# Kernel tuning notes

Hardware: AMD Instinct MI355X
Metric: run time of the kernel (lower is better)

The kernel has to match this reference:

```python
import jax, jax.numpy as jnp
from jax import lax
import numpy as np

T, B = 64, 32            # rollout length, num envs
IMG = 84                 # NatureCNN input size
POS_N = 10               # grid size per position axis
N_ACT = 5                # discrete actions
HID = 128                # LSTM hidden size
CNN_OUT = 512
IN_DIM = CNN_OUT + 2 * POS_N  # 532


def setup_inputs() -> dict:
    key = jax.random.key(0)
    ks = jax.random.split(key, 16)
    N = T * B
    s = 0.05  # weight scale to keep activations in sane range
    rn = lambda k, shp: jax.random.normal(k, shp, jnp.float32) * s
    return {
        "image": jax.random.uniform(ks[0], (N, IMG, IMG, 3), jnp.float32),
        "position": jax.random.randint(ks[1], (N, 2), 0, POS_N, jnp.int32),
        "done": jax.random.randint(ks[2], (N,), 0, 2, jnp.int32),
        "h0": jnp.zeros((B, 1, HID), jnp.float32),
        "c0": jnp.zeros((B, 1, HID), jnp.float32),
        "W1": rn(ks[3], (8, 8, 3, 32)),   "b1": jnp.zeros((32,), jnp.float32),
        "W2": rn(ks[4], (4, 4, 32, 64)),  "b2": jnp.zeros((64,), jnp.float32),
        "W3": rn(ks[5], (3, 3, 64, 64)),  "b3": jnp.zeros((64,), jnp.float32),
        "Wfc": rn(ks[6], (3136, CNN_OUT)), "bfc": jnp.zeros((CNN_OUT,), jnp.float32),
        "Wih": rn(ks[7], (4 * HID, IN_DIM)), "Whh": rn(ks[8], (4 * HID, HID)),
        "bih": jnp.zeros((4 * HID,), jnp.float32), "bhh": jnp.zeros((4 * HID,), jnp.float32),
        "Wp": rn(ks[9], (HID, N_ACT)), "bp": jnp.zeros((N_ACT,), jnp.float32),
        "Wv": rn(ks[10], (HID, 1)),    "bv": jnp.zeros((1,), jnp.float32),
    }


def _conv(x, w, b, stride):
    y = lax.conv_general_dilated(x, w, (stride, stride), 'VALID',
                                 dimension_numbers=('NHWC', 'HWIO', 'NHWC'))
    return jax.nn.relu(y + b)


def reference(image, position, done, h0, c0,
              W1, b1, W2, b2, W3, b3, Wfc, bfc,
              Wih, Whh, bih, bhh, Wp, bp, Wv, bv):
    # --- NatureCNN feature extractor ---
    x = _conv(image, W1, b1, 4)          # (N,20,20,32)
    x = _conv(x, W2, b2, 2)              # (N,9,9,64)
    x = _conv(x, W3, b3, 1)              # (N,7,7,64)
    x = x.reshape(x.shape[0], -1)        # (N,3136)
    feat = jax.nn.relu(x @ Wfc + bfc)    # (N,512)
    # --- one-hot position encoding ---
    oh = jnp.concatenate([jax.nn.one_hot(position[:, 0], POS_N, dtype=feat.dtype),
                          jax.nn.one_hot(position[:, 1], POS_N, dtype=feat.dtype)], axis=1)
    z = jnp.concatenate([feat, oh], axis=1).reshape(T, B, IN_DIM)
    d = done.astype(feat.dtype).reshape(T, B)
    # --- per-timestep masked LSTM scan with episode resets ---
    h = h0[:, 0, :]  # (B,HID), num_layers=1
    c = c0[:, 0, :]

    def step(carry, inp):
        h, c = carry
        x_t, d_t = inp
        m = (1.0 - d_t)[:, None]
        h = h * m
        c = c * m
        g = x_t @ Wih.T + bih + h @ Whh.T + bhh          # (B,4*HID)
        i, f, gg, o = jnp.split(g, 4, axis=1)             # torch gate order i,f,g,o
        i = jax.nn.sigmoid(i)
        f = jax.nn.sigmoid(f)
        o = jax.nn.sigmoid(o)
        c = f * c + i * jnp.tanh(gg)
        h = o * jnp.tanh(c)
        return (h, c), h

    (h, c), hs = lax.scan(step, (h, c), (z, d))
    H = hs.reshape(T * B, HID)
    logits = H @ Wp + bp                 # (N, N_ACT) -> Categorical logits
    v = H @ Wv + bv                      # (N, 1)
    return logits, v, h[:, None, :], c[:, None, :]
```

## Files before the change

kernel.cpp:

```cpp
#include <hip/hip_runtime.h>

typedef unsigned short ushort_t;
typedef unsigned int uint_t;
typedef __attribute__((ext_vector_type(8))) short short8;
typedef __attribute__((ext_vector_type(4))) short short4v;
typedef __attribute__((ext_vector_type(4))) float floatx4;

__device__ __forceinline__ float bf2f(ushort_t u){
    union { uint_t i; float f; } c; c.i = ((uint_t)u) << 16; return c.f;
}
__device__ __forceinline__ ushort_t f2bf(float x){
    union { float f; uint_t i; } c; c.f = x;
    uint_t i = c.i;
    return (ushort_t)((i + 0x7fffu + ((i >> 16) & 1u)) >> 16);
}
__device__ __forceinline__ uint_t cvt2fast(float a, float b){
    union { float f; uint_t i; } ca, cb; ca.f = a; cb.f = b;
    uint_t ia = ca.i + 0x8000u, ib = cb.i + 0x8000u;
    return __builtin_amdgcn_perm(ib, ia, 0x07060302u);
}
__device__ __forceinline__ short8 lds_load8(const ushort_t* p){
    union { short4v h[2]; short8 s; } u;
    u.h[0] = *(const short4v*)p;
    u.h[1] = *(const short4v*)(p + 4);
    return u.s;
}
__device__ __forceinline__ float relu_f(float x){ return fmaxf(x, 0.0f); }
__device__ __forceinline__ float sigmoid_f(float x){ return 1.0f / (1.0f + __expf(-x)); }

#define NT 2048
#define TT 64

__global__ __launch_bounds__(256) void prep_kernel(
    const float* __restrict__ Wih, ushort_t* __restrict__ Wihb)
{
    int i = blockIdx.x * 256 + threadIdx.x;
    int j = i >> 9, k = i & 511;
    Wihb[i] = f2bf(Wih[j * 532 + k]);
}

__global__ __launch_bounds__(256) void prep_convw_kernel(
    const float* __restrict__ W1, const float* __restrict__ W2,
    const float* __restrict__ W3, ushort_t* __restrict__ W1b,
    ushort_t* __restrict__ W2b, ushort_t* __restrict__ W3b)
{
    int i = blockIdx.x * 256 + threadIdx.x;
    if (i < 8192) {
        int ky = i >> 10, oc = (i >> 5) & 31, k = i & 31;
        float v = 0.0f;
        if (k < 24) { int kx = k / 3, ic = k % 3; v = W1[((ky * 8 + kx) * 3 + ic) * 32 + oc]; }
        W1b[i] = f2bf(v);
        return;
    }
    i -= 8192;
    if (i < 32768) {
        int kk = i >> 11, oc = (i >> 5) & 63, ic = i & 31;
        W2b[i] = f2bf(W2[(kk * 32 + ic) * 64 + oc]);
        return;
    }
    i -= 32768;
    if (i < 36864) {
        int p = i >> 12, oc = (i >> 6) & 63, ic = i & 63;
        W3b[i] = f2bf(W3[(p * 64 + ic) * 64 + oc]);
    }
}

__global__ __launch_bounds__(256) void wfct_kernel(
    const float* __restrict__ Wfc, ushort_t* __restrict__ WfcT)
{
    __shared__ ushort_t t_s[64][65];
    int kb = blockIdx.x % 49, jb = blockIdx.x / 49;
    int k0 = kb * 64, j0 = jb * 64;
    int jj = threadIdx.x & 63, i4 = threadIdx.x >> 6;
    for (int rr = i4; rr < 64; rr += 4)
        t_s[rr][jj] = f2bf(Wfc[(size_t)(k0 + rr) * 512 + j0 + jj]);
    __syncthreads();
    for (int rr = i4; rr < 64; rr += 4)
        WfcT[(size_t)(j0 + rr) * 3136 + k0 + jj] = t_s[jj][rr];
}

__global__ __launch_bounds__(256) void convs_mfma(
    const float* __restrict__ img,
    const ushort_t* __restrict__ W1b, const float* __restrict__ b1,
    const ushort_t* __restrict__ W2b, const float* __restrict__ b2,
    const ushort_t* __restrict__ W3b, const float* __restrict__ b3,
    ushort_t* __restrict__ out3)
{
    __shared__ ushort_t smem[35576];
    ushort_t* c1_s  = smem;
    ushort_t* img_s = smem + 14400;
    ushort_t* c2_s  = smem + 14400;

    int n = blockIdx.x, tid = threadIdx.x;
    int w = tid >> 6, lane = tid & 63;
    int r = lane & 15, q = lane >> 4;

    const float4* ip = (const float4*)(img + (size_t)n * 21168);
    for (int i = tid; i < 5292; i += 256) {
        float4 v = ip[i];
        uint_t lo = cvt2fast(v.x, v.y);
        uint_t hi = cvt2fast(v.z, v.w);
        *(uint2*)(img_s + i * 4) = make_uint2(lo, hi);
    }
    if (tid < 8) img_s[21168 + tid] = 0;
    __syncthreads();

    {
        int oct = w & 1;
        short8 bf[8];
        #pragma unroll
        for (int ky = 0; ky < 8; ky++)
            bf[ky] = *(const short8*)(W1b + (ky * 32 + oct * 16 + r) * 32 + q * 8);
        float bb = b1[oct * 16 + r];
        for (int t = (w >> 1); t < 25; t += 2) {
            int pxa = t * 16 + r;
            int oy = pxa / 20, ox = pxa % 20;
            floatx4 acc = {0.f, 0.f, 0.f, 0.f};
            #pragma unroll
            for (int ky = 0; ky < 8; ky++) {
                short8 a = lds_load8(img_s + ((oy * 4 + ky) * 84 + ox * 4) * 3 + q * 8);
                acc = __builtin_amdgcn_mfma_f32_16x16x32_bf16(a, bf[ky], acc, 0, 0, 0);
            }
            int pxs = t * 16 + q * 4;
            #pragma unroll
            for (int i = 0; i < 4; i++)
                c1_s[(pxs + i) * 36 + oct * 16 + r] = f2bf(relu_f(acc[i] + bb));
        }
    }
    __syncthreads();

    {
        int oct = w;
        short8 bfr[16];
        #pragma unroll
        for (int kk = 0; kk < 16; kk++)
            bfr[kk] = *(const short8*)(W2b + (kk * 64 + oct * 16 + r) * 32 + q * 8);
        float bb = b2[oct * 16 + r];
        for (int t = 0; t < 6; t++) {
            int pxa = min(t * 16 + r, 80);
            int oy = pxa / 9, ox = pxa % 9;
            floatx4 acc = {0.f, 0.f, 0.f, 0.f};
            #pragma unroll
            for (int ky = 0; ky < 4; ky++) {
                #pragma unroll
                for (int kx = 0; kx < 4; kx++) {
                    int qin = (oy * 2 + ky) * 20 + ox * 2 + kx;
                    short8 a = lds_load8(c1_s + qin * 36 + q * 8);
                    acc = __builtin_amdgcn_mfma_f32_16x16x32_bf16(a, bfr[ky * 4 + kx], acc, 0, 0, 0);
                }
            }
            #pragma unroll
            for (int i = 0; i < 4; i++) {
                int px = t * 16 + q * 4 + i;
                if (px < 81)
                    c2_s[px * 68 + oct * 16 + r] = f2bf(relu_f(acc[i] + bb));
            }
        }
    }
    __syncthreads();

    {
        int oct = w;
        short8 bfr[18];
        #pragma unroll
        for (int p = 0; p < 9; p++) {
            #pragma unroll
            for (int h = 0; h < 2; h++)
                bfr[p * 2 + h] = *(const short8*)(W3b + (p * 64 + oct * 16 + r) * 64 + h * 32 + q * 8);
        }
        float bb = b3[oct * 16 + r];
        for (int t = 0; t < 4; t++) {
            int pxa = min(t * 16 + r, 48);
            int oy = pxa / 7, ox = pxa % 7;
            floatx4 acc = {0.f, 0.f, 0.f, 0.f};
            #pragma unroll
            for (int ky = 0; ky < 3; ky++) {
                #pragma unroll
                for (int kx = 0; kx < 3; kx++) {
                    int qin = (oy + ky) * 9 + ox + kx;
                    const ushort_t* ap = c2_s + qin * 68 + q * 8;
                    short8 a0 = lds_load8(ap);
                    short8 a1 = lds_load8(ap + 32);
                    acc = __builtin_amdgcn_mfma_f32_16x16x32_bf16(a0, bfr[(ky * 3 + kx) * 2],     acc, 0, 0, 0);
                    acc = __builtin_amdgcn_mfma_f32_16x16x32_bf16(a1, bfr[(ky * 3 + kx) * 2 + 1], acc, 0, 0, 0);
                }
            }
            #pragma unroll
            for (int i = 0; i < 4; i++) {
                int px = t * 16 + q * 4 + i;
                if (px < 49)
                    out3[(size_t)n * 3136 + px * 64 + oct * 16 + r] = f2bf(relu_f(acc[i] + bb));
            }
        }
    }
}

__global__ __launch_bounds__(256) void fc_mfma_kernel(
    const ushort_t* __restrict__ A, const ushort_t* __restrict__ BT,
    const float* __restrict__ bfc, ushort_t* __restrict__ feat)
{
    int mb = blockIdx.x & 63, nb = blockIdx.x >> 6;
    int tid = threadIdx.x;
    int w = tid >> 6, lane = tid & 63;
    int r = lane & 15, q = lane >> 4;
    int m0 = mb * 32 + (w & 1) * 16;
    int n0 = nb * 64 + (w >> 1) * 32;
    const ushort_t* arow  = A  + (size_t)(m0 + r) * 3136 + q * 8;
    const ushort_t* brow0 = BT + (size_t)(n0 + r) * 3136 + q * 8;
    const ushort_t* brow1 = BT + (size_t)(n0 + 16 + r) * 3136 + q * 8;
    floatx4 acc0 = {0.f, 0.f, 0.f, 0.f}, acc1 = {0.f, 0.f, 0.f, 0.f};
    short8 a  = *(const short8*)arow;
    short8 b0 = *(const short8*)brow0;
    short8 b1 = *(const short8*)brow1;
    for (int kk = 1; kk < 98; kk++) {
        short8 an  = *(const short8*)(arow  + kk * 32);
        short8 b0n = *(const short8*)(brow0 + kk * 32);
        short8 b1n = *(const short8*)(brow1 + kk * 32);
        acc0 = __builtin_amdgcn_mfma_f32_16x16x32_bf16(a, b0, acc0, 0, 0, 0);
        acc1 = __builtin_amdgcn_mfma_f32_16x16x32_bf16(a, b1, acc1, 0, 0, 0);
        a = an; b0 = b0n; b1 = b1n;
    }
    acc0 = __builtin_amdgcn_mfma_f32_16x16x32_bf16(a, b0, acc0, 0, 0, 0);
    acc1 = __builtin_amdgcn_mfma_f32_16x16x32_bf16(a, b1, acc1, 0, 0, 0);
    int c0 = n0 + r, c1 = n0 + 16 + r;
    float bb0 = bfc[c0], bb1 = bfc[c1];
    #pragma unroll
    for (int i = 0; i < 4; i++) {
        int row = m0 + q * 4 + i;
        feat[(size_t)row * 512 + c0] = f2bf(relu_f(acc0[i] + bb0));
        feat[(size_t)row * 512 + c1] = f2bf(relu_f(acc1[i] + bb1));
    }
}

__global__ __launch_bounds__(256) void gates_mfma_kernel(
    const ushort_t* __restrict__ A, const ushort_t* __restrict__ Wihb,
    const float* __restrict__ Wih, const float* __restrict__ bih,
    const float* __restrict__ bhh, const int* __restrict__ pos,
    float* __restrict__ gx)
{
    int mb = blockIdx.x & 63, nb = blockIdx.x >> 6;
    int tid = threadIdx.x;
    int w = tid >> 6, lane = tid & 63;
    int r = lane & 15, q = lane >> 4;
    int m0 = mb * 32 + (w & 1) * 16;
    int n0 = nb * 64 + (w >> 1) * 32;
    const ushort_t* arow  = A    + (size_t)(m0 + r) * 512 + q * 8;
    const ushort_t* brow0 = Wihb + (size_t)(n0 + r) * 512 + q * 8;
    const ushort_t* brow1 = Wihb + (size_t)(n0 + 16 + r) * 512 + q * 8;
    floatx4 acc0 = {0.f, 0.f, 0.f, 0.f}, acc1 = {0.f, 0.f, 0.f, 0.f};
    short8 a  = *(const short8*)arow;
    short8 b0 = *(const short8*)brow0;
    short8 b1 = *(const short8*)brow1;
    for (int kk = 1; kk < 16; kk++) {
        short8 an  = *(const short8*)(arow  + kk * 32);
        short8 b0n = *(const short8*)(brow0 + kk * 32);
        short8 b1n = *(const short8*)(brow1 + kk * 32);
        acc0 = __builtin_amdgcn_mfma_f32_16x16x32_bf16(a, b0, acc0, 0, 0, 0);
        acc1 = __builtin_amdgcn_mfma_f32_16x16x32_bf16(a, b1, acc1, 0, 0, 0);
        a = an; b0 = b0n; b1 = b1n;
    }
    acc0 = __builtin_amdgcn_mfma_f32_16x16x32_bf16(a, b0, acc0, 0, 0, 0);
    acc1 = __builtin_amdgcn_mfma_f32_16x16x32_bf16(a, b1, acc1, 0, 0, 0);
    int j0 = n0 + r, j1 = n0 + 16 + r;
    float bias0 = bih[j0] + bhh[j0];
    float bias1 = bih[j1] + bhh[j1];
    #pragma unroll
    for (int i = 0; i < 4; i++) {
        int row = m0 + q * 4 + i;
        int p0 = pos[2 * row], p1 = pos[2 * row + 1];
        float oh0 = Wih[(size_t)j0 * 532 + 512 + p0] + Wih[(size_t)j0 * 532 + 522 + p1];
        float oh1 = Wih[(size_t)j1 * 532 + 512 + p0] + Wih[(size_t)j1 * 532 + 522 + p1];
        gx[(size_t)row * 512 + j0] = acc0[i] + bias0 + oh0;
        gx[(size_t)row * 512 + j1] = acc1[i] + bias1 + oh1;
    }
}

__global__ __launch_bounds__(512, 2) void lstm_kernel(
    const float* __restrict__ gx, const float* __restrict__ Whh,
    const int* __restrict__ done, const float* __restrict__ h0,
    const float* __restrict__ c0, ushort_t* __restrict__ hs,
    float* __restrict__ out)
{
    __shared__ __align__(16) float h_s[128];
    __shared__ float gates_s[512];
    int b = blockIdx.x, tid = threadIdx.x;
    int g = tid >> 7, j = tid & 127;

    float w[128];
    const float* wr = Whh + (size_t)(g * 128 + j) * 128;
    #pragma unroll
    for (int k = 0; k < 128; k += 4) {
        float4 v = *(const float4*)(wr + k);
        w[k] = v.x; w[k + 1] = v.y; w[k + 2] = v.z; w[k + 3] = v.w;
    }
    float h = h0[b * 128 + j];
    float c = c0[b * 128 + j];
    const float* gxb = gx + (size_t)b * 512;

    for (int t = 0; t < TT; t++) {
        float m = 1.0f - (float)done[t * 32 + b];
        c *= m;
        if (g == 0) h_s[j] = h * m;
        __syncthreads();
        float acc = 0.0f;
        #pragma unroll
        for (int k = 0; k < 128; k += 4) {
            float4 hv = *(const float4*)&h_s[k];
            acc = fmaf(w[k], hv.x, acc);
            acc = fmaf(w[k + 1], hv.y, acc);
            acc = fmaf(w[k + 2], hv.z, acc);
            acc = fmaf(w[k + 3], hv.w, acc);
        }
        acc += gxb[(size_t)t * 32 * 512 + (g << 7) + j];
        gates_s[(g << 7) + j] = acc;
        __syncthreads();
        float iv = sigmoid_f(gates_s[j]);
        float fv = sigmoid_f(gates_s[128 + j]);
        float gv = tanhf(gates_s[256 + j]);
        float ov = sigmoid_f(gates_s[384 + j]);
        c = fv * c + iv * gv;
        h = ov * tanhf(c);
        if (g == 0) hs[((size_t)t * 32 + b) * 128 + j] = f2bf(h);
    }
    if (g == 0) {
        out[12288 + b * 128 + j] = h;
        out[16384 + b * 128 + j] = c;
    }
}

__global__ __launch_bounds__(256) void heads_kernel(
    const ushort_t* __restrict__ hs, const float* __restrict__ Wp,
    const float* __restrict__ bp, const float* __restrict__ Wv,
    const float* __restrict__ bv, float* __restrict__ out)
{
    int id = blockIdx.x * 256 + threadIdx.x;
    int n = id / 6, q = id % 6;
    const ushort_t* hrow = hs + (size_t)n * 128;
    if (q < 5) {
        float acc = bp[q];
        for (int k = 0; k < 128; k++) acc = fmaf(bf2f(hrow[k]), Wp[k * 5 + q], acc);
        out[n * 5 + q] = acc;
    } else {
        float acc = bv[0];
        for (int k = 0; k < 128; k++) acc = fmaf(bf2f(hrow[k]), Wv[k], acc);
        out[10240 + n] = acc;
    }
}

extern "C" void kernel_launch(void* const* d_in, const int* in_sizes, int n_in,
                              void* d_out, int out_size, void* d_ws, size_t ws_size,
                              hipStream_t stream) {
    const float* image = (const float*)d_in[0];
    const int*   pos   = (const int*)d_in[1];
    const int*   done  = (const int*)d_in[2];
    const float* h0    = (const float*)d_in[3];
    const float* c0    = (const float*)d_in[4];
    const float* W1    = (const float*)d_in[5];
    const float* b1    = (const float*)d_in[6];
    const float* W2    = (const float*)d_in[7];
    const float* b2    = (const float*)d_in[8];
    const float* W3    = (const float*)d_in[9];
    const float* b3    = (const float*)d_in[10];
    const float* Wfc   = (const float*)d_in[11];
    const float* bfc   = (const float*)d_in[12];
    const float* Wih   = (const float*)d_in[13];
    const float* Whh   = (const float*)d_in[14];
    const float* bih   = (const float*)d_in[15];
    const float* bhh   = (const float*)d_in[16];
    const float* Wp    = (const float*)d_in[17];
    const float* bp    = (const float*)d_in[18];
    const float* Wv    = (const float*)d_in[19];
    const float* bv    = (const float*)d_in[20];

    char* ws = (char*)d_ws;
    ushort_t* Wihb = (ushort_t*)(ws + 0);
    ushort_t* WfcT = (ushort_t*)(ws + 524288);
    ushort_t* W1b  = (ushort_t*)(ws + 3735552);
    ushort_t* W2b  = (ushort_t*)(ws + 3751936);
    ushort_t* W3b  = (ushort_t*)(ws + 3817472);
    ushort_t* out3 = (ushort_t*)(ws + 4194304);
    ushort_t* feat = (ushort_t*)(ws + 17039360);
    float*    gx   = (float*)(ws + 19136512);
    ushort_t* hs   = (ushort_t*)(ws + 23330816);

    float* out = (float*)d_out;

    prep_kernel<<<1024, 256, 0, stream>>>(Wih, Wihb);
    prep_convw_kernel<<<304, 256, 0, stream>>>(W1, W2, W3, W1b, W2b, W3b);
    wfct_kernel<<<392, 256, 0, stream>>>(Wfc, WfcT);
    convs_mfma<<<2048, 256, 0, stream>>>(image, W1b, b1, W2b, b2, W3b, b3, out3);
    fc_mfma_kernel<<<512, 256, 0, stream>>>(out3, WfcT, bfc, feat);
    gates_mfma_kernel<<<512, 256, 0, stream>>>(feat, Wihb, Wih, bih, bhh, pos, gx);
    lstm_kernel<<<32, 512, 0, stream>>>(gx, Whh, done, h0, c0, hs, out);
    heads_kernel<<<48, 256, 0, stream>>>(hs, Wp, bp, Wv, bv, out);
}
```

Before: 539.1 us.

## Read conv1 image patches straight from global memory, drop LDS image staging

The conv1 stage no longer stages the whole fp32 image into shared memory as bf16. Each wave now loads its 8x24 patch rows directly from global memory and converts them in registers. Each wave computes both 16-channel output halves, so the tile loop is split across 4 waves instead of 2, and lanes with q==3 feed zeros where they previously read the padded tail. Removing the large image buffer shrinks shared memory, and launch bounds now request 4 blocks per CU to raise occupancy. The trade-off is more redundant, uncoalesced global reads, since overlapping patches are re-read by many lanes.

Result: no change. 536.5 us (-0.5%).

```diff
diff --git a/kernel.cpp b/kernel.cpp
--- a/kernel.cpp
+++ b/kernel.cpp
@@ -79,52 +79,56 @@
         WfcT[(size_t)(j0 + rr) * 3136 + k0 + jj] = t_s[jj][rr];
 }
 
-__global__ __launch_bounds__(256) void convs_mfma(
+__global__ __launch_bounds__(256, 4) void convs_mfma(
     const float* __restrict__ img,
     const ushort_t* __restrict__ W1b, const float* __restrict__ b1,
     const ushort_t* __restrict__ W2b, const float* __restrict__ b2,
     const ushort_t* __restrict__ W3b, const float* __restrict__ b3,
     ushort_t* __restrict__ out3)
 {
-    __shared__ ushort_t smem[35576];
-    ushort_t* c1_s  = smem;
-    ushort_t* img_s = smem + 14400;
-    ushort_t* c2_s  = smem + 14400;
+    __shared__ ushort_t c1_s[400 * 36];
+    __shared__ ushort_t c2_s[81 * 68];
 
     int n = blockIdx.x, tid = threadIdx.x;
     int w = tid >> 6, lane = tid & 63;
     int r = lane & 15, q = lane >> 4;
 
-    const float4* ip = (const float4*)(img + (size_t)n * 21168);
-    for (int i = tid; i < 5292; i += 256) {
-        float4 v = ip[i];
-        uint_t lo = cvt2fast(v.x, v.y);
-        uint_t hi = cvt2fast(v.z, v.w);
-        *(uint2*)(img_s + i * 4) = make_uint2(lo, hi);
-    }
-    if (tid < 8) img_s[21168 + tid] = 0;
-    __syncthreads();
-
     {
-        int oct = w & 1;
-        short8 bf[8];
+        short8 bf0[8], bf1[8];
         #pragma unroll
-        for (int ky = 0; ky < 8; ky++)
-            bf[ky] = *(const short8*)(W1b + (ky * 32 + oct * 16 + r) * 32 + q * 8);
-        float bb = b1[oct * 16 + r];
-        for (int t = (w >> 1); t < 25; t += 2) {
+        for (int ky = 0; ky < 8; ky++) {
+            bf0[ky] = *(const short8*)(W1b + (ky * 32 +      r) * 32 + q * 8);
+            bf1[ky] = *(const short8*)(W1b + (ky * 32 + 16 + r) * 32 + q * 8);
+        }
+        float bb0 = b1[r], bb1 = b1[16 + r];
+        const float* abase = img + (size_t)n * 21168;
+        for (int t = w; t < 25; t += 4) {
             int pxa = t * 16 + r;
             int oy = pxa / 20, ox = pxa % 20;
-            floatx4 acc = {0.f, 0.f, 0.f, 0.f};
+            floatx4 acc0 = {0.f, 0.f, 0.f, 0.f}, acc1 = {0.f, 0.f, 0.f, 0.f};
             #pragma unroll
             for (int ky = 0; ky < 8; ky++) {
-                short8 a = lds_load8(img_s + ((oy * 4 + ky) * 84 + ox * 4) * 3 + q * 8);
-                acc = __builtin_amdgcn_mfma_f32_16x16x32_bf16(a, bf[ky], acc, 0, 0, 0);
+                short8 a = {0,0,0,0,0,0,0,0};
+                if (q < 3) {
+                    const float* p = abase + ((oy * 4 + ky) * 84 + ox * 4) * 3 + q * 8;
+                    float4 f0 = *(const float4*)p;
+                    float4 f1 = *(const float4*)(p + 4);
+                    union { uint_t u[4]; short8 s; } pk;
+                    pk.u[0] = cvt2fast(f0.x, f0.y);
+                    pk.u[1] = cvt2fast(f0.z, f0.w);
+                    pk.u[2] = cvt2fast(f1.x, f1.y);
+                    pk.u[3] = cvt2fast(f1.z, f1.w);
+                    a = pk.s;
+                }
+                acc0 = __builtin_amdgcn_mfma_f32_16x16x32_bf16(a, bf0[ky], acc0, 0, 0, 0);
+                acc1 = __builtin_amdgcn_mfma_f32_16x16x32_bf16(a, bf1[ky], acc1, 0, 0, 0);
             }
             int pxs = t * 16 + q * 4;
             #pragma unroll
-            for (int i = 0; i < 4; i++)
-                c1_s[(pxs + i) * 36 + oct * 16 + r] = f2bf(relu_f(acc[i] + bb));
+            for (int i = 0; i < 4; i++) {
+                c1_s[(pxs + i) * 36 +      r] = f2bf(relu_f(acc0[i] + bb0));
+                c1_s[(pxs + i) * 36 + 16 + r] = f2bf(relu_f(acc1[i] + bb1));
+            }
         }
     }
     __syncthreads();
```
